# Optimization experiments

Measured on AMD Instinct MI355X. Metric: run time of the kernel, lower is better.

Reference implementation:

```python
import jax, jax.numpy as jnp
import numpy as np

B, S, D = 8, 2048, 512
H, LAT, OUT = 8, 64, 64


def setup_inputs() -> dict:
    key = jax.random.key(0)
    ks = jax.random.split(key, 5)
    return {
        "x": jax.random.normal(ks[0], (B, S, D), dtype=jnp.float32),
        "WQ": jax.random.normal(ks[1], (H, D, LAT), dtype=jnp.float32) * 0.05,
        "WK": jax.random.normal(ks[2], (H, D, LAT), dtype=jnp.float32) * 0.05,
        "WV": jax.random.normal(ks[3], (H, D, OUT), dtype=jnp.float32) * 0.05,
        "WO": jax.random.normal(ks[4], (H * OUT, OUT), dtype=jnp.float32) * 0.05,
    }


def reference(x, WQ, WK, WV, WO):
    # Per-head projections, vectorized over heads (faithful to the TF python loop).
    Q = jnp.einsum('bsd,hdk->bhsk', x, WQ)   # [B,H,S,LAT]
    K = jnp.einsum('bsd,hdk->bhsk', x, WK)   # [B,H,S,LAT]
    V = jnp.einsum('bsd,hdo->bhso', x, WV)   # [B,H,S,OUT]
    scale = jnp.asarray(1.0 / np.sqrt(LAT), dtype=x.dtype)
    A = jnp.einsum('bhqk,bhsk->bhqs', Q, K) * scale  # [B,H,S,S]
    A = jax.nn.softmax(A, axis=-1)
    O = jnp.einsum('bhqs,bhso->bhqo', A, V)  # [B,H,S,OUT]
    # concat heads along last axis (head 0 first, matching the TF loop order)
    O = jnp.transpose(O, (0, 2, 1, 3)).reshape(x.shape[0], x.shape[1], H * OUT)
    return O @ WO  # [B,S,OUT]
```

## Files before the change

### kernel.cpp

```cpp
#include <hip/hip_runtime.h>
#include <hip/hip_bf16.h>
#include <math.h>

static constexpr int Bn = 8, Sn = 2048, Dn = 512, Hn = 8, LATn = 64, OUTn = 64;

typedef short  bf16x8 __attribute__((ext_vector_type(8)));
typedef float  f32x4  __attribute__((ext_vector_type(4)));

__device__ __forceinline__ unsigned short f2bf(float f) {
    union { float f; unsigned int i; } v; v.f = f;
    unsigned int x = v.i;
    return (unsigned short)((x + 0x7FFFu + ((x >> 16) & 1u)) >> 16);
}
__device__ __forceinline__ unsigned int pack2bf(float a, float b) {
    unsigned int ua = __float_as_uint(a) + 0x8000u;
    unsigned int ub = __float_as_uint(b) + 0x8000u;
    return (ua >> 16) | (ub & 0xFFFF0000u);
}
__device__ __forceinline__ unsigned int cvtpk(float a, float b) {
    unsigned int r;
    asm("v_cvt_pk_bf16_f32 %0, %1, %2" : "=v"(r) : "v"(a), "v"(b));
    return r;
}

#if __has_builtin(__builtin_amdgcn_exp2f)
#define EXP2(x) __builtin_amdgcn_exp2f(x)
#else
#define EXP2(x) exp2f(x)
#endif

__device__ __forceinline__ void gl_lds16(const void* g, void* l) {
    __builtin_amdgcn_global_load_lds(
        (const __attribute__((address_space(1))) unsigned int*)g,
        (__attribute__((address_space(3))) unsigned int*)l, 16, 0, 0);
}

__global__ __launch_bounds__(256) void wprep(
    const float* __restrict__ WQ, const float* __restrict__ WK,
    const float* __restrict__ WV, const float* __restrict__ WO,
    unsigned short* __restrict__ WT)
{
    __shared__ float tile[64][65];
    const int t  = threadIdx.x;
    const int d0 = blockIdx.x * 64;
    const int yy = blockIdx.y;

    const float* W; float scale = 1.0f; size_t dstbase;
    if (yy < 24) {
        int h = yy / 3, which = yy % 3;
        W = (which == 0) ? WQ : (which == 1) ? WK : WV;
        W += (size_t)h * Dn * 64;
        if (which == 0) scale = 0.125f * 1.44269504088896f;
        dstbase = ((size_t)h * 192 + which * 64) * Dn;
    } else {
        W = WO;
        dstbase = (size_t)8 * 192 * Dn;
    }

    for (int i = 0; i < 4; ++i) {
        int idx = i * 256 + t;
        int r = idx >> 4, c = (idx & 15) * 4;
        float4 u = *(const float4*)(W + (size_t)(d0 + r) * 64 + c);
        tile[r][c] = u.x; tile[r][c+1] = u.y; tile[r][c+2] = u.z; tile[r][c+3] = u.w;
    }
    __syncthreads();
    const int n = t & 63, dd = t >> 6;
    unsigned short pk[16];
    for (int i = 0; i < 16; ++i) pk[i] = f2bf(tile[dd*16 + i][n] * scale);
    size_t dst = dstbase + (size_t)n * Dn + d0 + dd * 16;
    *(bf16x8*)(WT + dst)     = *(bf16x8*)(pk);
    *(bf16x8*)(WT + dst + 8) = *(bf16x8*)(pk + 8);
}

__global__ __launch_bounds__(256) void qkv_mfma(
    const float* __restrict__ x, const unsigned short* __restrict__ WT,
    unsigned short* __restrict__ Qb, unsigned short* __restrict__ Kb,
    unsigned short* __restrict__ VT)
{
    __shared__ __align__(16) unsigned short lds[64*72 + 192*72];
    unsigned short* Xs = lds;
    unsigned short* Ws = lds + 64*72;
    unsigned short* L  = lds;

    const int t  = threadIdx.x;
    const int w  = t >> 6, ln = t & 63;
    const int nl = ln & 15, g = ln >> 4;
    const int bh = blockIdx.y, b = bh >> 3, h = bh & 7;
    const int s0 = blockIdx.x * 64;

    f32x4 acc[4][3];
    for (int m = 0; m < 4; ++m)
        for (int j = 0; j < 3; ++j) acc[m][j] = (f32x4){0.f, 0.f, 0.f, 0.f};

    for (int k0 = 0; k0 < Dn; k0 += 64) {
        __syncthreads();
        for (int i = 0; i < 2; ++i) {
            int idx = i * 256 + t;
            int r = idx >> 3, c = (idx & 7) * 8;
            const float* src = x + ((size_t)(b * Sn + s0 + r)) * Dn + k0 + c;
            float4 u0 = *(const float4*)(src);
            float4 u1 = *(const float4*)(src + 4);
            unsigned int pk[4] = { pack2bf(u0.x, u0.y), pack2bf(u0.z, u0.w),
                                   pack2bf(u1.x, u1.y), pack2bf(u1.z, u1.w) };
            *(bf16x8*)(Xs + r*72 + c) = *(bf16x8*)pk;
        }
        for (int i = 0; i < 6; ++i) {
            int idx = i * 256 + t;
            int r = idx >> 3, c = (idx & 7) * 8;
            *(bf16x8*)(Ws + r*72 + c) =
                *(const bf16x8*)(WT + ((size_t)h * 192 + r) * Dn + k0 + c);
        }
        __syncthreads();
        #pragma unroll
        for (int kc = 0; kc < 2; ++kc) {
            bf16x8 a[4], bb[3];
            for (int m = 0; m < 4; ++m)
                a[m]  = *(const bf16x8*)(Xs + (16*m + nl)*72 + 32*kc + 8*g);
            for (int j = 0; j < 3; ++j)
                bb[j] = *(const bf16x8*)(Ws + ((3*w + j)*16 + nl)*72 + 32*kc + 8*g);
            for (int m = 0; m < 4; ++m)
                for (int j = 0; j < 3; ++j)
                    acc[m][j] = __builtin_amdgcn_mfma_f32_16x16x32_bf16(
                                    a[m], bb[j], acc[m][j], 0, 0, 0);
        }
    }
    __syncthreads();
    for (int m = 0; m < 4; ++m)
        for (int j = 0; j < 3; ++j) {
            int n = 48*w + 16*j + nl;
            for (int r = 0; r < 4; ++r)
                L[(16*m + 4*g + r)*200 + n] = f2bf(acc[m][j][r]);
        }
    __syncthreads();
    for (int i = 0; i < 4; ++i) {
        int idx = i * 256 + t;
        int r = idx >> 4, c = (idx & 15) * 8;
        bf16x8 v = *(const bf16x8*)(L + r*200 + c);
        size_t o = ((size_t)bh * Sn + s0 + r) * 64;
        if (c < 64) *(bf16x8*)(Qb + o + c)      = v;
        else        *(bf16x8*)(Kb + o + c - 64) = v;
    }
    {
        int o = t & 63, cc = t >> 6;
        unsigned short pk[16];
        for (int i = 0; i < 16; ++i) {
            int srow = 32*(cc>>1) + 16*((i>>2)&1) + 8*(cc&1) + 4*((i>>3)&1) + (i&3);
            pk[i] = L[srow*200 + 128 + o];
        }
        size_t dst = ((size_t)bh * 64 + o) * Sn + s0 + 16*cc;
        *(bf16x8*)(VT + dst)     = *(bf16x8*)(pk);
        *(bf16x8*)(VT + dst + 8) = *(bf16x8*)(pk + 8);
    }
}

__global__ __launch_bounds__(512, 4) void flash_mfma(
    const unsigned short* __restrict__ Qb,
    const unsigned short* __restrict__ Kb,
    const unsigned short* __restrict__ VT,
    unsigned short* __restrict__ Ob)
{
    __shared__ __align__(16) unsigned short KV[3][2][4096];

    const int t  = threadIdx.x;
    const int w  = t >> 6, ln = t & 63;
    const int qh = ln & 15, g = (ln >> 4) & 3;
    const int bh = blockIdx.y, b = bh >> 3, h = bh & 7;
    const int q0 = blockIdx.x * 256;
    const int qw = q0 + 32 * w;

    bf16x8 bq[2][2];
    #pragma unroll
    for (int qs = 0; qs < 2; ++qs) {
        const unsigned short* qp =
            Qb + ((size_t)bh * Sn + qw + 16*qs + qh) * 64 + 8*g;
        bq[qs][0] = *(const bf16x8*)(qp);
        bq[qs][1] = *(const bf16x8*)(qp + 32);
    }

    const int r0 = t >> 3;
    const int cs = (t & 7) ^ (r0 & 7);
    const unsigned short* kg = Kb + ((size_t)bh * Sn + r0) * 64 + cs * 8;
    const unsigned short* vg = VT + ((size_t)bh * 64 + r0) * Sn + cs * 8;

    const int koff0 = qh*64 + (((g    ) ^ (qh & 7)) * 8);
    const int koff1 = qh*64 + (((4 + g) ^ (qh & 7)) * 8);

    f32x4 o_acc[2][4];
    #pragma unroll
    for (int qs = 0; qs < 2; ++qs)
        #pragma unroll
        for (int f = 0; f < 4; ++f) o_acc[qs][f] = (f32x4){0.f, 0.f, 0.f, 0.f};
    float l_run[2] = {0.f, 0.f};

    gl_lds16(kg,        &KV[0][0][w * 512]);
    gl_lds16(vg,        &KV[0][1][w * 512]);
    gl_lds16(kg + 4096, &KV[1][0][w * 512]);
    gl_lds16(vg + 64,   &KV[1][1][w * 512]);

    constexpr int NT = Sn / 64;
    int buf = 0, sbuf = 2;
    for (int kt = 0; kt < NT; ++kt) {
        if (kt < NT - 1) asm volatile("s_waitcnt vmcnt(2)" ::: "memory");
        else             asm volatile("s_waitcnt vmcnt(0)" ::: "memory");
        __builtin_amdgcn_s_barrier();

        if (kt < NT - 2) {
            gl_lds16(kg + (size_t)(kt + 2) * 4096, &KV[sbuf][0][w * 512]);
            gl_lds16(vg + (size_t)(kt + 2) * 64,   &KV[sbuf][1][w * 512]);
        }
        const unsigned short* Kt = KV[buf][0];
        const unsigned short* Vt = KV[buf][1];

        f32x4 st[2][4];
        #pragma unroll
        for (int qs = 0; qs < 2; ++qs)
            #pragma unroll
            for (int f = 0; f < 4; ++f) st[qs][f] = (f32x4){0.f, 0.f, 0.f, 0.f};
        __builtin_amdgcn_s_setprio(1);
        #pragma unroll
        for (int kc = 0; kc < 2; ++kc) {
            const int ko = kc ? koff1 : koff0;
            bf16x8 a0 = *(const bf16x8*)(Kt + ko);
            bf16x8 a1 = *(const bf16x8*)(Kt + ko + 1024);
            bf16x8 a2 = *(const bf16x8*)(Kt + ko + 2048);
            bf16x8 a3 = *(const bf16x8*)(Kt + ko + 3072);
            #pragma unroll
            for (int qs = 0; qs < 2; ++qs) {
                st[qs][0] = __builtin_amdgcn_mfma_f32_16x16x32_bf16(a0, bq[qs][kc], st[qs][0], 0, 0, 0);
                st[qs][1] = __builtin_amdgcn_mfma_f32_16x16x32_bf16(a1, bq[qs][kc], st[qs][1], 0, 0, 0);
                st[qs][2] = __builtin_amdgcn_mfma_f32_16x16x32_bf16(a2, bq[qs][kc], st[qs][2], 0, 0, 0);
                st[qs][3] = __builtin_amdgcn_mfma_f32_16x16x32_bf16(a3, bq[qs][kc], st[qs][3], 0, 0, 0);
            }
        }
        __builtin_amdgcn_s_setprio(0);

        bf16x8 bp[2][2];
        #pragma unroll
        for (int qs = 0; qs < 2; ++qs) {
            float e0[4], e1[4], e2[4], e3[4];
            #pragma unroll
            for (int r = 0; r < 4; ++r) {
                e0[r] = EXP2(st[qs][0][r]);
                e1[r] = EXP2(st[qs][1][r]);
                e2[r] = EXP2(st[qs][2][r]);
                e3[r] = EXP2(st[qs][3][r]);
            }
            l_run[qs] += ((e0[0]+e0[1])+(e0[2]+e0[3])) + ((e1[0]+e1[1])+(e1[2]+e1[3]))
                       + ((e2[0]+e2[1])+(e2[2]+e2[3])) + ((e3[0]+e3[1])+(e3[2]+e3[3]));
            unsigned int p0[4] = { cvtpk(e0[0],e0[1]), cvtpk(e0[2],e0[3]),
                                   cvtpk(e1[0],e1[1]), cvtpk(e1[2],e1[3]) };
            unsigned int p1[4] = { cvtpk(e2[0],e2[1]), cvtpk(e2[2],e2[3]),
                                   cvtpk(e3[0],e3[1]), cvtpk(e3[2],e3[3]) };
            bp[qs][0] = *(bf16x8*)p0;
            bp[qs][1] = *(bf16x8*)p1;
        }

        __builtin_amdgcn_s_setprio(1);
        #pragma unroll
        for (int kc = 0; kc < 2; ++kc) {
            const int ko = kc ? koff1 : koff0;
            bf16x8 v0 = *(const bf16x8*)(Vt + ko);
            bf16x8 v1 = *(const bf16x8*)(Vt + ko + 1024);
            bf16x8 v2 = *(const bf16x8*)(Vt + ko + 2048);
            bf16x8 v3 = *(const bf16x8*)(Vt + ko + 3072);
            #pragma unroll
            for (int qs = 0; qs < 2; ++qs) {
                o_acc[qs][0] = __builtin_amdgcn_mfma_f32_16x16x32_bf16(v0, bp[qs][kc], o_acc[qs][0], 0, 0, 0);
                o_acc[qs][1] = __builtin_amdgcn_mfma_f32_16x16x32_bf16(v1, bp[qs][kc], o_acc[qs][1], 0, 0, 0);
                o_acc[qs][2] = __builtin_amdgcn_mfma_f32_16x16x32_bf16(v2, bp[qs][kc], o_acc[qs][2], 0, 0, 0);
                o_acc[qs][3] = __builtin_amdgcn_mfma_f32_16x16x32_bf16(v3, bp[qs][kc], o_acc[qs][3], 0, 0, 0);
            }
        }
        __builtin_amdgcn_s_setprio(0);

        buf  = (buf  == 2) ? 0 : buf  + 1;
        sbuf = (sbuf == 2) ? 0 : sbuf + 1;
    }

    #pragma unroll
    for (int qs = 0; qs < 2; ++qs) {
        l_run[qs] += __shfl_xor(l_run[qs], 16);
        l_run[qs] += __shfl_xor(l_run[qs], 32);
    }

    #pragma unroll
    for (int qs = 0; qs < 2; ++qs) {
        float inv_l = 1.f / l_run[qs];
        unsigned short* op = Ob
            + ((size_t)(b * Sn + q0 + 32*w + 16*qs + qh)) * 512 + h*64 + 4*g;
        #pragma unroll
        for (int f = 0; f < 4; ++f) {
            unsigned int lo = cvtpk(o_acc[qs][f][0] * inv_l, o_acc[qs][f][1] * inv_l);
            unsigned int hi = cvtpk(o_acc[qs][f][2] * inv_l, o_acc[qs][f][3] * inv_l);
            *(uint2*)(op + 16*f) = make_uint2(lo, hi);
        }
    }
}

__global__ __launch_bounds__(256) void out_mfma(
    const unsigned short* __restrict__ Ob, const unsigned short* __restrict__ WOT,
    float* __restrict__ out)
{
    __shared__ __align__(16) unsigned short As[64 * 72];
    __shared__ __align__(16) unsigned short Bs[64 * 72];

    const int t  = threadIdx.x;
    const int w  = t >> 6, ln = t & 63;
    const int qh = ln & 15, g = ln >> 4;
    const int bs0 = blockIdx.x * 64;

    f32x4 acc[4];
    for (int n = 0; n < 4; ++n) acc[n] = (f32x4){0.f, 0.f, 0.f, 0.f};

    for (int k0 = 0; k0 < 512; k0 += 64) {
        __syncthreads();
        for (int i = 0; i < 2; ++i) {
            int idx = i * 256 + t;
            int r = idx >> 3, c = (idx & 7) * 8;
            *(bf16x8*)(As + r*72 + c) =
                *(const bf16x8*)(Ob + ((size_t)(bs0 + r)) * 512 + k0 + c);
            *(bf16x8*)(Bs + r*72 + c) =
                *(const bf16x8*)(WOT + (size_t)r * Dn + k0 + c);
        }
        __syncthreads();
        #pragma unroll
        for (int kc = 0; kc < 2; ++kc) {
            bf16x8 a = *(const bf16x8*)(As + (16*w + qh)*72 + 32*kc + 8*g);
            #pragma unroll
            for (int n = 0; n < 4; ++n) {
                bf16x8 bb = *(const bf16x8*)(Bs + (16*n + qh)*72 + 32*kc + 8*g);
                acc[n] = __builtin_amdgcn_mfma_f32_16x16x32_bf16(a, bb, acc[n], 0, 0, 0);
            }
        }
    }
    for (int n = 0; n < 4; ++n)
        for (int r = 0; r < 4; ++r)
            out[((size_t)(bs0 + 16*w + 4*g + r)) * 64 + 16*n + qh] = acc[n][r];
}

extern "C" void kernel_launch(void* const* d_in, const int* in_sizes, int n_in,
                              void* d_out, int out_size, void* d_ws, size_t ws_size,
                              hipStream_t stream)
{
    const float* x  = (const float*)d_in[0];
    const float* WQ = (const float*)d_in[1];
    const float* WK = (const float*)d_in[2];
    const float* WV = (const float*)d_in[3];
    const float* WO = (const float*)d_in[4];
    float* out = (float*)d_out;

    const size_t NQ = (size_t)Bn * Hn * Sn * LATn;
    char* p = (char*)d_ws;
    unsigned short* Qb  = (unsigned short*)p;           p += NQ * 2;
    unsigned short* Kb  = (unsigned short*)p;           p += NQ * 2;
    unsigned short* VT  = (unsigned short*)p;           p += NQ * 2;
    unsigned short* WT  = (unsigned short*)p;           p += ((size_t)Hn*192*Dn + 64*Dn) * 2;
    unsigned short* Ob  = (unsigned short*)p;
    unsigned short* WOT = WT + (size_t)Hn * 192 * Dn;

    wprep     <<<dim3(8, 25),         256, 0, stream>>>(WQ, WK, WV, WO, WT);
    qkv_mfma  <<<dim3(Sn/64, Bn*Hn),  256, 0, stream>>>(x, WT, Qb, Kb, VT);
    flash_mfma<<<dim3(Sn/256, Bn*Hn), 512, 0, stream>>>(Qb, Kb, VT, Ob);
    out_mfma  <<<dim3(Bn*Sn/64),      256, 0, stream>>>(Ob, WOT, out);
}
```

Baseline: 205.5 us.

## Pre-convert x to bf16 and double-buffer QKV projection with direct LDS loads

Adds an xprep kernel that converts x to bf16 once into a workspace buffer that aliases Ob, instead of each of the 8 head blocks reconverting the fp32 input. qkv_mfma now streams the bf16 x tiles into swizzled, double-buffered LDS using global_load_lds, and reads weight fragments straight from global memory into registers rather than staging them in LDS. The goal is to cut the redundant fp32 reads of x and overlap loads with MFMA work. The cost is an extra kernel launch and an extra pass over x, with weight reads now hitting L2 per wave.

```diff
diff --git a/kernel.cpp b/kernel.cpp
--- a/kernel.cpp
+++ b/kernel.cpp
@@ -33,6 +33,23 @@
     __builtin_amdgcn_global_load_lds(
         (const __attribute__((address_space(1))) unsigned int*)g,
         (__attribute__((address_space(3))) unsigned int*)l, 16, 0, 0);
+}
+
+__global__ __launch_bounds__(256) void xprep(
+    const float* __restrict__ x, unsigned short* __restrict__ Xb)
+{
+    const size_t base = ((size_t)blockIdx.x * 256 + threadIdx.x) * 16;
+    const float* src = x + base;
+    float4 u0 = *(const float4*)(src);
+    float4 u1 = *(const float4*)(src + 4);
+    float4 u2 = *(const float4*)(src + 8);
+    float4 u3 = *(const float4*)(src + 12);
+    unsigned int pk[8] = { pack2bf(u0.x,u0.y), pack2bf(u0.z,u0.w),
+                           pack2bf(u1.x,u1.y), pack2bf(u1.z,u1.w),
+                           pack2bf(u2.x,u2.y), pack2bf(u2.z,u2.w),
+                           pack2bf(u3.x,u3.y), pack2bf(u3.z,u3.w) };
+    *(bf16x8*)(Xb + base)     = *(bf16x8*)(pk);
+    *(bf16x8*)(Xb + base + 8) = *(bf16x8*)(pk + 4);
 }
 
 __global__ __launch_bounds__(256) void wprep(
@@ -72,15 +89,13 @@
     *(bf16x8*)(WT + dst + 8) = *(bf16x8*)(pk + 8);
 }
 
-__global__ __launch_bounds__(256) void qkv_mfma(
-    const float* __restrict__ x, const unsigned short* __restrict__ WT,
+__global__ __launch_bounds__(256, 4) void qkv_mfma(
+    const unsigned short* __restrict__ Xb, const unsigned short* __restrict__ WT,
     unsigned short* __restrict__ Qb, unsigned short* __restrict__ Kb,
     unsigned short* __restrict__ VT)
 {
-    __shared__ __align__(16) unsigned short lds[64*72 + 192*72];
-    unsigned short* Xs = lds;
-    unsigned short* Ws = lds + 64*72;
-    unsigned short* L  = lds;
+    __shared__ __align__(16) unsigned short lds[64 * 200];
+    unsigned short* L = lds;
 
     const int t  = threadIdx.x;
     const int w  = t >> 6, ln = t & 63;
@@ -88,40 +103,53 @@
     const int bh = blockIdx.y, b = bh >> 3, h = bh & 7;
     const int s0 = blockIdx.x * 64;
 
+    const int r0 = t >> 3,      sc0 = (t & 7) ^ (r0 & 7);
+    const int r1 = 32 + (t>>3), sc1 = (t & 7) ^ (r1 & 7);
+    const unsigned short* xg0 = Xb + ((size_t)(b * Sn + s0 + r0)) * Dn + sc0 * 8;
+    const unsigned short* xg1 = Xb + ((size_t)(b * Sn + s0 + r1)) * Dn + sc1 * 8;
+
+    const int p = nl & 7;
+    const int aoff0 = nl * 64 + 8 * ((g    ) ^ p);
+    const int aoff1 = nl * 64 + 8 * ((4 + g) ^ p);
+
+    const unsigned short* wb = WT + ((size_t)h * 192 + 48 * w + nl) * Dn + 8 * g;
+
     f32x4 acc[4][3];
     for (int m = 0; m < 4; ++m)
         for (int j = 0; j < 3; ++j) acc[m][j] = (f32x4){0.f, 0.f, 0.f, 0.f};
 
-    for (int k0 = 0; k0 < Dn; k0 += 64) {
-        __syncthreads();
-        for (int i = 0; i < 2; ++i) {
-            int idx = i * 256 + t;
-            int r = idx >> 3, c = (idx & 7) * 8;
-            const float* src = x + ((size_t)(b * Sn + s0 + r)) * Dn + k0 + c;
-            float4 u0 = *(const float4*)(src);
-            float4 u1 = *(const float4*)(src + 4);
-            unsigned int pk[4] = { pack2bf(u0.x, u0.y), pack2bf(u0.z, u0.w),
-                                   pack2bf(u1.x, u1.y), pack2bf(u1.z, u1.w) };
-            *(bf16x8*)(Xs + r*72 + c) = *(bf16x8*)pk;
-        }
-        for (int i = 0; i < 6; ++i) {
-            int idx = i * 256 + t;
-            int r = idx >> 3, c = (idx & 7) * 8;
-            *(bf16x8*)(Ws + r*72 + c) =
-                *(const bf16x8*)(WT + ((size_t)h * 192 + r) * Dn + k0 + c);
-        }
-        __syncthreads();
+    gl_lds16(xg0, lds + 512 * w);
+    gl_lds16(xg1, lds + 2048 + 512 * w);
+
+    for (int kt = 0; kt < 8; ++kt) {
+        asm volatile("s_waitcnt vmcnt(0)" ::: "memory");
+        __builtin_amdgcn_s_barrier();
+        if (kt < 7) {
+            unsigned short* dst = lds + 4096 * ((kt + 1) & 1);
+            gl_lds16(xg0 + (kt + 1) * 64, dst + 512 * w);
+            gl_lds16(xg1 + (kt + 1) * 64, dst + 2048 + 512 * w);
+        }
+        const unsigned short* cur = lds + 4096 * (kt & 1);
+        const int k0 = kt * 64;
+
+        bf16x8 bb[3][2];
+        #pragma unroll
+        for (int j = 0; j < 3; ++j) {
+            bb[j][0] = *(const bf16x8*)(wb + j * 8192 + k0);
+            bb[j][1] = *(const bf16x8*)(wb + j * 8192 + k0 + 32);
+        }
         #pragma unroll
         for (int kc = 0; kc < 2; ++kc) {
-            bf16x8 a[4], bb[3];
+            bf16x8 a[4];
+            #pragma unroll
             for (int m = 0; m < 4; ++m)
-                a[m]  = *(const bf16x8*)(Xs + (16*m + nl)*72 + 32*kc + 8*g);
-            for (int j = 0; j < 3; ++j)
-                bb[j] = *(const bf16x8*)(Ws + ((3*w + j)*16 + nl)*72 + 32*kc + 8*g);
+                a[m] = *(const bf16x8*)(cur + (kc ? aoff1 : aoff0) + m * 1024);
+            #pragma unroll
             for (int m = 0; m < 4; ++m)
+                #pragma unroll
                 for (int j = 0; j < 3; ++j)
                     acc[m][j] = __builtin_amdgcn_mfma_f32_16x16x32_bf16(
-                                    a[m], bb[j], acc[m][j], 0, 0, 0);
+                                    a[m], bb[j][kc], acc[m][j], 0, 0, 0);
         }
     }
     __syncthreads();
@@ -357,9 +385,11 @@
     unsigned short* WT  = (unsigned short*)p;           p += ((size_t)Hn*192*Dn + 64*Dn) * 2;
     unsigned short* Ob  = (unsigned short*)p;
     unsigned short* WOT = WT + (size_t)Hn * 192 * Dn;
-
+    unsigned short* Xb  = Ob;
+
+    xprep     <<<dim3(2048),          256, 0, stream>>>(x, Xb);
     wprep     <<<dim3(8, 25),         256, 0, stream>>>(WQ, WK, WV, WO, WT);
-    qkv_mfma  <<<dim3(Sn/64, Bn*Hn),  256, 0, stream>>>(x, WT, Qb, Kb, VT);
+    qkv_mfma  <<<dim3(Sn/64, Bn*Hn),  256, 0, stream>>>(Xb, WT, Qb, Kb, VT);
     flash_mfma<<<dim3(Sn/256, Bn*Hn), 512, 0, stream>>>(Qb, Kb, VT, Ob);
     out_mfma  <<<dim3(Bn*Sn/64),      256, 0, stream>>>(Ob, WOT, out);
 }
```

After: 219.1 us. 1.07x slower.
